# Optimization experiments

Hardware: AMD Instinct MI355X
Metric: run time of the kernel (lower is better)

Reference implementation:

```python
import jax, jax.numpy as jnp
import numpy as np

B, NX, NY, CIN = 4, 128, 128, 64
D, H = 64, 8  # out_channels, nhead
EPS = 1e-5


def setup_inputs() -> dict:
    key = jax.random.key(0)
    ks = jax.random.split(key, 12)
    s_in = 1.0 / np.sqrt(CIN)
    s_hd = 1.0 / np.sqrt(H * D)
    return {
        "v": jax.random.normal(ks[0], (B, NX, NY, CIN), jnp.float32),
        "Wq_w": jax.random.uniform(ks[1], (CIN, H * D), jnp.float32, -s_in, s_in),
        "Wq_b": jax.random.uniform(ks[2], (H * D,), jnp.float32, -s_in, s_in),
        "Wk_w": jax.random.uniform(ks[3], (CIN, H * D), jnp.float32, -s_in, s_in),
        "Wk_b": jax.random.uniform(ks[4], (H * D,), jnp.float32, -s_in, s_in),
        "Wv_w": jax.random.uniform(ks[5], (CIN, H * D), jnp.float32, -s_in, s_in),
        "Wv_b": jax.random.uniform(ks[6], (H * D,), jnp.float32, -s_in, s_in),
        "lnq_g": jnp.ones((H, D), jnp.float32),
        "lnq_b": jnp.zeros((H, D), jnp.float32),
        "lnk_g": jnp.ones((H, D), jnp.float32),
        "lnk_b": jnp.zeros((H, D), jnp.float32),
        "Wo_w": jax.random.uniform(ks[7], (H * D, D), jnp.float32, -s_hd, s_hd),
        "Wo_b": jax.random.uniform(ks[8], (D,), jnp.float32, -s_hd, s_hd),
    }


def _layernorm(x, gamma, beta):
    # x: [b,h,n,d]; gamma/beta: [h,d] (per-head params)
    mu = jnp.mean(x, axis=-1, keepdims=True)
    var = jnp.mean(jnp.square(x - mu), axis=-1, keepdims=True)
    xn = (x - mu) * jax.lax.rsqrt(var + EPS)
    return xn * gamma[None, :, None, :] + beta[None, :, None, :]


def reference(v, Wq_w, Wq_b, Wk_w, Wk_b, Wv_w, Wv_b,
              lnq_g, lnq_b, lnk_g, lnk_b, Wo_w, Wo_b):
    b, nx, ny, _ = v.shape
    n = nx * ny
    vf = v.reshape(b, n, -1)  # [b, n, cin]
    # QKV projections -> [b, h, n, d]
    def proj(w, bias):
        y = vf @ w + bias  # [b, n, h*d]
        return y.reshape(b, n, H, D).transpose(0, 2, 1, 3)
    Q = _layernorm(proj(Wq_w, Wq_b), lnq_g, lnq_b)
    K = _layernorm(proj(Wk_w, Wk_b), lnk_g, lnk_b)
    V = proj(Wv_w, Wv_b)
    # Non-softmax linear attention: (Q K^T) V == Q (K^T V); use O(n d^2) form
    kv = jnp.einsum('bhnd,bhne->bhde', K, V)      # [b,h,d,d]
    attn = jnp.einsum('bhmd,bhde->bhme', Q, kv)   # [b,h,n,d]
    attn = attn.transpose(0, 2, 1, 3).reshape(b, n, H * D)
    out = (attn @ Wo_w + Wo_b) / n
    return out.reshape(b, nx, ny, D)
```

## Files before the change

kernel.cpp:

```cpp
#include <hip/hip_runtime.h>
#include <hip/hip_bf16.h>

typedef __attribute__((ext_vector_type(8))) short bhalf8;
typedef __attribute__((ext_vector_type(4))) float f32x4;

#define MFMA_BF16 __builtin_amdgcn_mfma_f32_16x16x32_bf16

namespace {

constexpr int   NPIX  = 16384;
constexpr int   NCH   = 64;
constexpr int   TILE  = 66 * 64;
constexpr float EPSV  = 1e-5f;
constexpr float INV64 = 1.0f / 64.0f;
constexpr float INV_N = 1.0f / 16384.0f;

__device__ __forceinline__ unsigned short f2bf(float f) {
    unsigned int u = __builtin_bit_cast(unsigned int, f);
    u += 0x7fffu + ((u >> 16) & 1u);
    return (unsigned short)(u >> 16);
}

union B8 { bhalf8 v; unsigned int u[4]; };

__device__ __forceinline__ unsigned int pk2(float a, float b) {
    union { __hip_bfloat162 h; unsigned int u; } x;
    x.h = __float22bfloat162_rn(float2{a, b});
    return x.u;
}

__global__ void kpack(const float* __restrict__ Wk, const float* __restrict__ Wv,
                      const float* __restrict__ Wq,
                      unsigned short* __restrict__ wkpk, unsigned short* __restrict__ wvpk,
                      unsigned short* __restrict__ wqpk, unsigned short* __restrict__ wksumb,
                      float* __restrict__ cbeta)
{
    const int w = blockIdx.x >> 3, h = blockIdx.x & 7, t = threadIdx.x;
    const float* W = (w == 0) ? Wk : (w == 1) ? Wv : Wq;
    unsigned short* dst = (w == 0) ? wkpk : (w == 1) ? wvpk : wqpk;

    if (blockIdx.x == 0) cbeta[t] = 0.f;

#pragma unroll
    for (int i = 0; i < 2; ++i) {
        const int f = t * 2 + i;
        const int nt = (f >> 7) & 3, ks = (f >> 6) & 1, l = f & 63;
        const int g = l >> 4, m = l & 15;
        unsigned short tmp[8];
#pragma unroll
        for (int j = 0; j < 8; ++j)
            tmp[j] = f2bf(W[(size_t)(32 * ks + 8 * g + j) * 512 + h * 64 + 16 * nt + m]);
        unsigned short* d = dst + ((size_t)((h * 4 + nt) * 2 + ks)) * 512 + l * 8;
        *reinterpret_cast<ushort4*>(d)     = make_ushort4(tmp[0], tmp[1], tmp[2], tmp[3]);
        *reinterpret_cast<ushort4*>(d + 4) = make_ushort4(tmp[4], tmp[5], tmp[6], tmp[7]);
    }
    if (w == 0 && t < 64) {
        float s = 0.f;
        const float* row = Wk + (size_t)t * 512 + h * 64;
#pragma unroll
        for (int d = 0; d < 64; ++d) s += row[d];
        wksumb[h * 64 + t] = f2bf(s);
    }
}

__global__ __launch_bounds__(512, 2)
void ka_kv(const float* __restrict__ v,
           const unsigned short* __restrict__ wkpk, const unsigned short* __restrict__ wvpk,
           const unsigned short* __restrict__ wksumb,
           const float* __restrict__ bk, const float* __restrict__ bv,
           float* __restrict__ part)
{
    const int ch = blockIdx.x, b = blockIdx.y;
    const int t = threadIdx.x, h = t >> 6, l = t & 63, g = l >> 4, m16 = l & 15;

    __shared__ uint4 vlds4[2048];
    unsigned short* vlds = reinterpret_cast<unsigned short*>(vlds4);

    const float* vbase = v + ((size_t)b * NPIX + ch * 256) * 64;
#pragma unroll
    for (int i = 0; i < 4; ++i) {
        const int G = t + 512 * i;
        const int s = G >> 8, f = (G >> 6) & 3, ll = G & 63;
        const int mt = f >> 1, ks = f & 1, gg = ll >> 4, mm = ll & 15;
        const float* src = vbase + (size_t)(s * 32 + 16 * mt + mm) * 64 + 32 * ks + 8 * gg;
        const float4 a = *reinterpret_cast<const float4*>(src);
        const float4 c = *reinterpret_cast<const float4*>(src + 4);
        vlds4[G] = uint4{pk2(a.x, a.y), pk2(a.z, a.w), pk2(c.x, c.y), pk2(c.z, c.w)};
    }

    bhalf8 wkB[4][2], wvB[4][2], wks[2];
#pragma unroll
    for (int nt = 0; nt < 4; ++nt)
#pragma unroll
      for (int ks = 0; ks < 2; ++ks) {
          wkB[nt][ks] = *reinterpret_cast<const bhalf8*>(
              wkpk + ((size_t)((h * 4 + nt) * 2 + ks)) * 512 + l * 8);
          wvB[nt][ks] = *reinterpret_cast<const bhalf8*>(
              wvpk + ((size_t)((h * 4 + nt) * 2 + ks)) * 512 + l * 8);
      }
#pragma unroll
    for (int ks = 0; ks < 2; ++ks)
        wks[ks] = *reinterpret_cast<const bhalf8*>(wksumb + h * 64 + 32 * ks + 8 * g);

    float bksum;
    {
        float bl = bk[h * 64 + l];
#pragma unroll
        for (int m = 1; m < 64; m <<= 1) bl += __shfl_xor(bl, m, 64);
        bksum = bl;
    }
    float bkv[4], bvv[4];
#pragma unroll
    for (int nt = 0; nt < 4; ++nt) {
        bkv[nt] = bk[h * 64 + 16 * nt + m16];
        bvv[nt] = bv[h * 64 + 16 * nt + m16];
    }

    f32x4 kv[4][4];
#pragma unroll
    for (int i = 0; i < 4; ++i)
#pragma unroll
      for (int j = 0; j < 4; ++j) kv[i][j] = f32x4{0.f, 0.f, 0.f, 0.f};
    float tl[4] = {0.f, 0.f, 0.f, 0.f};
    float sv[4] = {0.f, 0.f, 0.f, 0.f};

    __syncthreads();

    for (int s = 0; s < 8; ++s) {
        bhalf8 vA[2][2];
#pragma unroll
        for (int mt = 0; mt < 2; ++mt)
#pragma unroll
          for (int ks = 0; ks < 2; ++ks)
            vA[mt][ks] = *reinterpret_cast<const bhalf8*>(
                vlds + ((size_t)(s * 4 + mt * 2 + ks) * 64 + l) * 8);

        f32x4 kq[2][4];
#pragma unroll
        for (int mt = 0; mt < 2; ++mt)
#pragma unroll
          for (int nt = 0; nt < 4; ++nt) {
              f32x4 a = {0.f, 0.f, 0.f, 0.f};
              a = MFMA_BF16(vA[mt][0], wkB[nt][0], a, 0, 0, 0);
              a = MFMA_BF16(vA[mt][1], wkB[nt][1], a, 0, 0, 0);
#pragma unroll
              for (int q = 0; q < 4; ++q) a[q] += bkv[nt];
              kq[mt][nt] = a;
          }
        f32x4 st[2];
#pragma unroll
        for (int mt = 0; mt < 2; ++mt) {
            f32x4 a = {0.f, 0.f, 0.f, 0.f};
            a = MFMA_BF16(vA[mt][0], wks[0], a, 0, 0, 0);
            a = MFMA_BF16(vA[mt][1], wks[1], a, 0, 0, 0);
            st[mt] = a;
        }
        f32x4 s2p[2];
#pragma unroll
        for (int mt = 0; mt < 2; ++mt)
#pragma unroll
          for (int q = 0; q < 4; ++q) {
              float acc = kq[mt][0][q] * kq[mt][0][q];
              acc = fmaf(kq[mt][1][q], kq[mt][1][q], acc);
              acc = fmaf(kq[mt][2][q], kq[mt][2][q], acc);
              acc = fmaf(kq[mt][3][q], kq[mt][3][q], acc);
              s2p[mt][q] = acc;
          }
#pragma unroll
        for (int mt = 0; mt < 2; ++mt)
#pragma unroll
          for (int q = 0; q < 4; ++q) {
              float x = s2p[mt][q];
              x += __shfl_xor(x, 1, 64);
              x += __shfl_xor(x, 2, 64);
              x += __shfl_xor(x, 4, 64);
              x += __shfl_xor(x, 8, 64);
              s2p[mt][q] = x;
          }
        f32x4 rsv[2], cmu[2];
#pragma unroll
        for (int mt = 0; mt < 2; ++mt)
#pragma unroll
          for (int q = 0; q < 4; ++q) {
              const float mu  = (st[mt][q] + bksum) * INV64;
              const float var = s2p[mt][q] * INV64 - mu * mu;
              const float rs  = rsqrtf(fmaxf(var, 0.f) + EPSV);
              rsv[mt][q] = rs;
              cmu[mt][q] = mu * rs;
          }
        B8 ka[4];
#pragma unroll
        for (int MT = 0; MT < 4; ++MT) {
            ka[MT].u[0] = pk2(kq[0][MT][0] * rsv[0][0], kq[0][MT][1] * rsv[0][1]);
            ka[MT].u[1] = pk2(kq[0][MT][2] * rsv[0][2], kq[0][MT][3] * rsv[0][3]);
            ka[MT].u[2] = pk2(kq[1][MT][0] * rsv[1][0], kq[1][MT][1] * rsv[1][1]);
            ka[MT].u[3] = pk2(kq[1][MT][2] * rsv[1][2], kq[1][MT][3] * rsv[1][3]);
        }
        f32x4 vq[2][4];
#pragma unroll
        for (int mt = 0; mt < 2; ++mt)
#pragma unroll
          for (int nt = 0; nt < 4; ++nt) {
              f32x4 a = {0.f, 0.f, 0.f, 0.f};
              a = MFMA_BF16(vA[mt][0], wvB[nt][0], a, 0, 0, 0);
              a = MFMA_BF16(vA[mt][1], wvB[nt][1], a, 0, 0, 0);
#pragma unroll
              for (int q = 0; q < 4; ++q) a[q] += bvv[nt];
              vq[mt][nt] = a;
          }
#pragma unroll
        for (int nt = 0; nt < 4; ++nt) {
            float acc = tl[nt], acc2 = sv[nt];
#pragma unroll
            for (int mt = 0; mt < 2; ++mt)
#pragma unroll
              for (int q = 0; q < 4; ++q) {
                  acc  = fmaf(cmu[mt][q], vq[mt][nt][q], acc);
                  acc2 += vq[mt][nt][q];
              }
            tl[nt] = acc; sv[nt] = acc2;
        }
        B8 vb[4];
#pragma unroll
        for (int NT = 0; NT < 4; ++NT) {
            vb[NT].u[0] = pk2(vq[0][NT][0], vq[0][NT][1]);
            vb[NT].u[1] = pk2(vq[0][NT][2], vq[0][NT][3]);
            vb[NT].u[2] = pk2(vq[1][NT][0], vq[1][NT][1]);
            vb[NT].u[3] = pk2(vq[1][NT][2], vq[1][NT][3]);
        }
#pragma unroll
        for (int MT = 0; MT < 4; ++MT)
#pragma unroll
          for (int NT = 0; NT < 4; ++NT)
              kv[MT][NT] = MFMA_BF16(ka[MT].v, vb[NT].v, kv[MT][NT], 0, 0, 0);
    }

#pragma unroll
    for (int nt = 0; nt < 4; ++nt) {
        float x = tl[nt];
        x += __shfl_xor(x, 16, 64); x += __shfl_xor(x, 32, 64);
        tl[nt] = x;
        float y = sv[nt];
        y += __shfl_xor(y, 16, 64); y += __shfl_xor(y, 32, 64);
        sv[nt] = y;
    }
    float* pdst = part + ((size_t)((b * NCH + ch) * 8 + h)) * TILE;
#pragma unroll
    for (int MT = 0; MT < 4; ++MT)
#pragma unroll
      for (int NT = 0; NT < 4; ++NT)
#pragma unroll
        for (int q = 0; q < 4; ++q)
            pdst[(16 * MT + 4 * g + q) * 64 + 16 * NT + m16] = kv[MT][NT][q];
    if (g == 0) {
#pragma unroll
        for (int nt = 0; nt < 4; ++nt) {
            pdst[64 * 64 + 16 * nt + m16] = tl[nt];
            pdst[65 * 64 + 16 * nt + m16] = sv[nt];
        }
    }
}

__global__ void k2a_reduce(const float* __restrict__ part, float* __restrict__ s2buf)
{
    const int seg = blockIdx.x, bh = blockIdx.y, t = threadIdx.x;
    const int b = bh >> 3, hh = bh & 7;
    const float* base = part + ((size_t)((b * NCH + seg * 8) * 8 + hh)) * TILE;
    float* dst = s2buf + ((size_t)(bh * 8 + seg)) * TILE;
#pragma unroll
    for (int k = 0; k < 5; ++k) {
        const int idx = t + k * 256;
        if (idx < TILE / 4) {
            float4 s = make_float4(0.f, 0.f, 0.f, 0.f);
#pragma unroll
            for (int i = 0; i < 8; ++i) {
                const float4 x = *reinterpret_cast<const float4*>(
                    base + (size_t)i * 8 * TILE + idx * 4);
                s.x += x.x; s.y += x.y; s.z += x.z; s.w += x.w;
            }
            *reinterpret_cast<float4*>(dst + idx * 4) = s;
        }
    }
}

__global__ void k2b_mix(const float* __restrict__ s2buf,
                        const float* __restrict__ lnkg, const float* __restrict__ lnkb,
                        const float* __restrict__ lnqg, const float* __restrict__ lnqb,
                        const float* __restrict__ Wo,   const float* __restrict__ Wob,
                        unsigned short* __restrict__ mpk, float* __restrict__ cbeta)
{
    const int h = blockIdx.x, b = blockIdx.y, t = threadIdx.x;
    __shared__ float kvs[64][65], wos[64][65], mls[64][65], Svs[64], tds[64], us[64];
    const int r = t >> 2, c0 = (t & 3) * 16;
    const float* sb = s2buf + ((size_t)((b * 8 + h) * 8)) * TILE;

    float acc[16];
#pragma unroll
    for (int i = 0; i < 16; ++i) acc[i] = 0.f;
#pragma unroll
    for (int seg = 0; seg < 8; ++seg) {
        const float* src = sb + (size_t)seg * TILE + r * 64 + c0;
#pragma unroll
        for (int q = 0; q < 4; ++q) {
            const float4 x = *reinterpret_cast<const float4*>(src + 4 * q);
            acc[4*q+0] += x.x; acc[4*q+1] += x.y; acc[4*q+2] += x.z; acc[4*q+3] += x.w;
        }
    }
#pragma unroll
    for (int i = 0; i < 16; ++i) kvs[r][c0 + i] = acc[i];

    if (t < 64) {
        float s = 0.f, s2 = 0.f;
#pragma unroll
        for (int seg = 0; seg < 8; ++seg) {
            s  += sb[(size_t)seg * TILE + 64 * 64 + t];
            s2 += sb[(size_t)seg * TILE + 65 * 64 + t];
        }
        tds[t] = s; Svs[t] = s2;
    }
#pragma unroll
    for (int i = 0; i < 16; i += 4) {
        const float4 x = *reinterpret_cast<const float4*>(
            Wo + ((size_t)(h * 64) + r) * 64 + c0 + i);
        wos[r][c0+i] = x.x; wos[r][c0+i+1] = x.y; wos[r][c0+i+2] = x.z; wos[r][c0+i+3] = x.w;
    }
    __syncthreads();
    {
        const float gk = lnkg[h * 64 + r], bk2 = lnkb[h * 64 + r];
#pragma unroll
        for (int i = 0; i < 16; ++i) {
            const int e = c0 + i;
            kvs[r][e] = gk * (kvs[r][e] - tds[e]) + bk2 * Svs[e];
        }
    }
    __syncthreads();
    if (t < 64) {
        float s = 0.f;
        for (int dd = 0; dd < 64; ++dd) s = fmaf(lnqb[h * 64 + dd], kvs[dd][t], s);
        us[t] = s;
    }
    float mrow[16];
#pragma unroll
    for (int i = 0; i < 16; ++i) mrow[i] = 0.f;
    for (int e2 = 0; e2 < 64; ++e2) {
        const float kr = kvs[r][e2];
#pragma unroll
        for (int i = 0; i < 16; ++i) mrow[i] = fmaf(kr, wos[e2][c0 + i], mrow[i]);
    }
    {
        const float gq = lnqg[h * 64 + r] * INV_N;
#pragma unroll
        for (int i = 0; i < 16; ++i) mls[r][c0 + i] = gq * mrow[i];
    }
    __syncthreads();
    if (t < 64) {
        float s = 0.f;
        for (int e2 = 0; e2 < 64; ++e2) s = fmaf(us[e2], wos[e2][t], s);
        atomicAdd(cbeta + b * 64 + t, s * INV_N);
        if (h == 0) atomicAdd(cbeta + b * 64 + t, Wob[t] * INV_N);
    }
#pragma unroll
    for (int i = 0; i < 2; ++i) {
        const int f = t * 2 + i;
        const int nt = (f >> 7) & 3, ks = (f >> 6) & 1, l = f & 63;
        const int g = l >> 4, m = l & 15;
        unsigned short o[8];
#pragma unroll
        for (int j = 0; j < 8; ++j) {
            const int d = 32 * ks + 16 * (j >> 2) + 4 * g + (j & 3);
            o[j] = f2bf(mls[d][16 * nt + m]);
        }
        unsigned short* dd = mpk + ((size_t)((b * 8 + h) * 8 + nt * 2 + ks)) * 512 + l * 8;
        *reinterpret_cast<ushort4*>(dd)     = make_ushort4(o[0], o[1], o[2], o[3]);
        *reinterpret_cast<ushort4*>(dd + 4) = make_ushort4(o[4], o[5], o[6], o[7]);
    }
}

__global__ __launch_bounds__(256, 2)
void k3_out(const float* __restrict__ v,
            const unsigned short* __restrict__ wqpk, const float* __restrict__ bq,
            const unsigned short* __restrict__ mpk,  const float* __restrict__ cbeta,
            float* __restrict__ out)
{
    const int blk = blockIdx.x, b = blockIdx.y;
    const int t = threadIdx.x, w = t >> 6, l = t & 63, g = l >> 4, m16 = l & 15;
    const size_t px0 = (size_t)b * NPIX + blk * 128 + w * 32;

    B8 vB[2][2];
#pragma unroll
    for (int nt = 0; nt < 2; ++nt)
#pragma unroll
      for (int ks = 0; ks < 2; ++ks) {
          const float* src = v + (px0 + 16 * nt + m16) * 64 + 32 * ks + 8 * g;
          const float4 a = *reinterpret_cast<const float4*>(src);
          const float4 c = *reinterpret_cast<const float4*>(src + 4);
          vB[nt][ks].u[0] = pk2(a.x, a.y); vB[nt][ks].u[1] = pk2(a.z, a.w);
          vB[nt][ks].u[2] = pk2(c.x, c.y); vB[nt][ks].u[3] = pk2(c.z, c.w);
      }
    float cbv[4];
#pragma unroll
    for (int nt = 0; nt < 4; ++nt) cbv[nt] = cbeta[b * 64 + 16 * nt + m16];

    f32x4 outa[2][4];
#pragma unroll
    for (int i = 0; i < 2; ++i)
#pragma unroll
      for (int j = 0; j < 4; ++j) outa[i][j] = f32x4{0.f, 0.f, 0.f, 0.f};

#pragma unroll
    for (int h = 0; h < 8; ++h) {
        bhalf8 wqA[4][2], mB[2][4];
#pragma unroll
        for (int mt = 0; mt < 4; ++mt)
#pragma unroll
          for (int ks = 0; ks < 2; ++ks)
            wqA[mt][ks] = *reinterpret_cast<const bhalf8*>(
                wqpk + ((size_t)((h * 4 + mt) * 2 + ks)) * 512 + l * 8);
#pragma unroll
        for (int ks = 0; ks < 2; ++ks)
#pragma unroll
          for (int nt = 0; nt < 4; ++nt)
            mB[ks][nt] = *reinterpret_cast<const bhalf8*>(
                mpk + ((size_t)((b * 8 + h) * 8 + nt * 2 + ks)) * 512 + l * 8);
        float4 bq4[4];
#pragma unroll
        for (int mt = 0; mt < 4; ++mt)
            bq4[mt] = *reinterpret_cast<const float4*>(bq + h * 64 + 16 * mt + 4 * g);

        f32x4 qa[4][2];
#pragma unroll
        for (int mt = 0; mt < 4; ++mt)
#pragma unroll
          for (int nt = 0; nt < 2; ++nt) {
              f32x4 a = {0.f, 0.f, 0.f, 0.f};
              a = MFMA_BF16(wqA[mt][0], vB[nt][0].v, a, 0, 0, 0);
              a = MFMA_BF16(wqA[mt][1], vB[nt][1].v, a, 0, 0, 0);
              a[0] += bq4[mt].x; a[1] += bq4[mt].y;
              a[2] += bq4[mt].z; a[3] += bq4[mt].w;
              qa[mt][nt] = a;
          }
        float mu[2], rs[2];
#pragma unroll
        for (int nt = 0; nt < 2; ++nt) {
            float s1 = 0.f, s2 = 0.f;
#pragma unroll
            for (int mt = 0; mt < 4; ++mt)
#pragma unroll
              for (int q = 0; q < 4; ++q) {
                  const float x = qa[mt][nt][q];
                  s1 += x; s2 = fmaf(x, x, s2);
              }
            s1 += __shfl_xor(s1, 16, 64); s1 += __shfl_xor(s1, 32, 64);
            s2 += __shfl_xor(s2, 16, 64); s2 += __shfl_xor(s2, 32, 64);
            mu[nt] = s1 * INV64;
            rs[nt] = rsqrtf(fmaxf(s2 * INV64 - mu[nt] * mu[nt], 0.f) + EPSV);
        }
        B8 ka[2][2];
#pragma unroll
        for (int MT = 0; MT < 2; ++MT)
#pragma unroll
          for (int ks = 0; ks < 2; ++ks) {
              ka[MT][ks].u[0] = pk2((qa[2*ks+0][MT][0] - mu[MT]) * rs[MT],
                                    (qa[2*ks+0][MT][1] - mu[MT]) * rs[MT]);
              ka[MT][ks].u[1] = pk2((qa[2*ks+0][MT][2] - mu[MT]) * rs[MT],
                                    (qa[2*ks+0][MT][3] - mu[MT]) * rs[MT]);
              ka[MT][ks].u[2] = pk2((qa[2*ks+1][MT][0] - mu[MT]) * rs[MT],
                                    (qa[2*ks+1][MT][1] - mu[MT]) * rs[MT]);
              ka[MT][ks].u[3] = pk2((qa[2*ks+1][MT][2] - mu[MT]) * rs[MT],
                                    (qa[2*ks+1][MT][3] - mu[MT]) * rs[MT]);
          }
#pragma unroll
        for (int MT = 0; MT < 2; ++MT)
#pragma unroll
          for (int nt = 0; nt < 4; ++nt) {
              outa[MT][nt] = MFMA_BF16(ka[MT][0].v, mB[0][nt], outa[MT][nt], 0, 0, 0);
              outa[MT][nt] = MFMA_BF16(ka[MT][1].v, mB[1][nt], outa[MT][nt], 0, 0, 0);
          }
    }

#pragma unroll
    for (int MT = 0; MT < 2; ++MT)
#pragma unroll
      for (int q = 0; q < 4; ++q) {
          float* orow = out + (px0 + 16 * MT + 4 * g + q) * 64;
#pragma unroll
          for (int nt = 0; nt < 4; ++nt)
              orow[16 * nt + m16] = outa[MT][nt][q] + cbv[nt];
      }
}

}

extern "C" void kernel_launch(void* const* d_in, const int* in_sizes, int n_in,
                              void* d_out, int out_size, void* d_ws, size_t ws_size,
                              hipStream_t stream)
{
    const float* v     = (const float*)d_in[0];
    const float* Wq_w  = (const float*)d_in[1];
    const float* Wq_b  = (const float*)d_in[2];
    const float* Wk_w  = (const float*)d_in[3];
    const float* Wk_b  = (const float*)d_in[4];
    const float* Wv_w  = (const float*)d_in[5];
    const float* Wv_b  = (const float*)d_in[6];
    const float* lnq_g = (const float*)d_in[7];
    const float* lnq_b = (const float*)d_in[8];
    const float* lnk_g = (const float*)d_in[9];
    const float* lnk_b = (const float*)d_in[10];
    const float* Wo_w  = (const float*)d_in[11];
    const float* Wo_b  = (const float*)d_in[12];
    float* out = (float*)d_out;

    float* wsf    = (float*)d_ws;
    float* part   = wsf;
    float* s2buf  = part + (size_t)4 * NCH * 8 * TILE;
    float* cbeta  = s2buf + (size_t)32 * 8 * TILE;
    unsigned short* base_s = (unsigned short*)(cbeta + 256);
    unsigned short* wkpk   = base_s;
    unsigned short* wvpk   = base_s + 32768;
    unsigned short* wqpk   = base_s + 65536;
    unsigned short* wksumb = base_s + 98304;
    unsigned short* mpk    = base_s + 98816;

    kpack<<<24, 256, 0, stream>>>(Wk_w, Wv_w, Wq_w, wkpk, wvpk, wqpk, wksumb, cbeta);
    ka_kv<<<dim3(NCH, 4), 512, 0, stream>>>(v, wkpk, wvpk, wksumb, Wk_b, Wv_b, part);
    k2a_reduce<<<dim3(8, 32), 256, 0, stream>>>(part, s2buf);
    k2b_mix<<<dim3(8, 4), 256, 0, stream>>>(s2buf, lnk_g, lnk_b, lnq_g, lnq_b,
                                            Wo_w, Wo_b, mpk, cbeta);
    k3_out<<<dim3(128, 4), 256, 0, stream>>>(v, wqpk, Wq_b, mpk, cbeta, out);
}
```

Before: 161.3 us.

## Fuse five kernel launches into one cooperative kernel with grid syncs

Merges the weight-packing, KV partial accumulation, reduction, mix and output stages into a single cooperative kernel of 256 blocks of 512 threads, separated by grid-wide barriers. This removes four kernel-launch gaps and the inter-kernel drain. The per-head bias contribution is now written to a per-(batch, head) buffer instead of being accumulated with atomics. In exchange, later stages run on a fixed grid of 256 blocks with 512 threads, which can reduce parallelism for stages such as the output pass that previously used 512 blocks of 256 threads. Each grid barrier also adds its own synchronisation cost.

```diff
diff --git a/kernel.cpp b/kernel.cpp
--- a/kernel.cpp
+++ b/kernel.cpp
@@ -1,5 +1,8 @@
 #include <hip/hip_runtime.h>
 #include <hip/hip_bf16.h>
+#include <hip/hip_cooperative_groups.h>
+
+namespace cg = cooperative_groups;
 
 typedef __attribute__((ext_vector_type(8))) short bhalf8;
 typedef __attribute__((ext_vector_type(4))) float f32x4;
@@ -29,464 +32,483 @@
     return x.u;
 }
 
-__global__ void kpack(const float* __restrict__ Wk, const float* __restrict__ Wv,
-                      const float* __restrict__ Wq,
-                      unsigned short* __restrict__ wkpk, unsigned short* __restrict__ wvpk,
-                      unsigned short* __restrict__ wqpk, unsigned short* __restrict__ wksumb,
-                      float* __restrict__ cbeta)
+__global__ __launch_bounds__(512, 2)
+void fused(const float* __restrict__ v,
+           const float* __restrict__ Wq, const float* __restrict__ bq,
+           const float* __restrict__ Wk, const float* __restrict__ bk,
+           const float* __restrict__ Wv, const float* __restrict__ bv,
+           const float* __restrict__ lnqg, const float* __restrict__ lnqb,
+           const float* __restrict__ lnkg, const float* __restrict__ lnkb,
+           const float* __restrict__ Wo,  const float* __restrict__ Wob,
+           float* __restrict__ out,
+           float* __restrict__ part, float* __restrict__ s2buf,
+           float* __restrict__ cbh,
+           unsigned short* __restrict__ wkpk, unsigned short* __restrict__ wvpk,
+           unsigned short* __restrict__ wqpk, unsigned short* __restrict__ wksumb,
+           unsigned short* __restrict__ mpk)
 {
-    const int w = blockIdx.x >> 3, h = blockIdx.x & 7, t = threadIdx.x;
-    const float* W = (w == 0) ? Wk : (w == 1) ? Wv : Wq;
-    unsigned short* dst = (w == 0) ? wkpk : (w == 1) ? wvpk : wqpk;
-
-    if (blockIdx.x == 0) cbeta[t] = 0.f;
-
-#pragma unroll
-    for (int i = 0; i < 2; ++i) {
-        const int f = t * 2 + i;
-        const int nt = (f >> 7) & 3, ks = (f >> 6) & 1, l = f & 63;
-        const int g = l >> 4, m = l & 15;
-        unsigned short tmp[8];
-#pragma unroll
-        for (int j = 0; j < 8; ++j)
-            tmp[j] = f2bf(W[(size_t)(32 * ks + 8 * g + j) * 512 + h * 64 + 16 * nt + m]);
-        unsigned short* d = dst + ((size_t)((h * 4 + nt) * 2 + ks)) * 512 + l * 8;
-        *reinterpret_cast<ushort4*>(d)     = make_ushort4(tmp[0], tmp[1], tmp[2], tmp[3]);
-        *reinterpret_cast<ushort4*>(d + 4) = make_ushort4(tmp[4], tmp[5], tmp[6], tmp[7]);
+    cg::grid_group grid = cg::this_grid();
+    const int bid = blockIdx.x, t = threadIdx.x;
+
+    __shared__ __align__(16) float smem[12864];
+
+    if (bid < 96) {
+        const int w = bid >> 5, sub = bid & 31, h = sub >> 2, nt = sub & 3;
+        const float* W = (w == 0) ? Wk : (w == 1) ? Wv : Wq;
+        unsigned short* dst = (w == 0) ? wkpk : (w == 1) ? wvpk : wqpk;
+        if (t < 128) {
+            const int ks = t >> 6, l = t & 63, g = l >> 4, m = l & 15;
+            unsigned short tmp[8];
+#pragma unroll
+            for (int j = 0; j < 8; ++j)
+                tmp[j] = f2bf(W[(size_t)(32 * ks + 8 * g + j) * 512 + h * 64 + 16 * nt + m]);
+            unsigned short* d = dst + ((size_t)((h * 4 + nt) * 2 + ks)) * 512 + l * 8;
+            *reinterpret_cast<ushort4*>(d)     = make_ushort4(tmp[0], tmp[1], tmp[2], tmp[3]);
+            *reinterpret_cast<ushort4*>(d + 4) = make_ushort4(tmp[4], tmp[5], tmp[6], tmp[7]);
+        }
+    } else if (bid < 104) {
+        const int h = bid - 96;
+        if (t < 64) {
+            float s = 0.f;
+            const float* row = Wk + (size_t)t * 512 + h * 64;
+#pragma unroll
+            for (int d = 0; d < 64; ++d) s += row[d];
+            wksumb[h * 64 + t] = f2bf(s);
+        }
     }
-    if (w == 0 && t < 64) {
-        float s = 0.f;
-        const float* row = Wk + (size_t)t * 512 + h * 64;
-#pragma unroll
-        for (int d = 0; d < 64; ++d) s += row[d];
-        wksumb[h * 64 + t] = f2bf(s);
+    __threadfence();
+    grid.sync();
+
+    {
+        const int b = bid >> 6, ch = bid & 63;
+        const int h = t >> 6, l = t & 63, g = l >> 4, m16 = l & 15;
+
+        uint4* vlds4 = reinterpret_cast<uint4*>(smem);
+        unsigned short* vlds = reinterpret_cast<unsigned short*>(smem);
+
+        const float* vbase = v + ((size_t)b * NPIX + ch * 256) * 64;
+#pragma unroll
+        for (int i = 0; i < 4; ++i) {
+            const int G = t + 512 * i;
+            const int s = G >> 8, f = (G >> 6) & 3, ll = G & 63;
+            const int mt = f >> 1, ks = f & 1, gg = ll >> 4, mm = ll & 15;
+            const float* src = vbase + (size_t)(s * 32 + 16 * mt + mm) * 64 + 32 * ks + 8 * gg;
+            const float4 a = *reinterpret_cast<const float4*>(src);
+            const float4 c = *reinterpret_cast<const float4*>(src + 4);
+            vlds4[G] = uint4{pk2(a.x, a.y), pk2(a.z, a.w), pk2(c.x, c.y), pk2(c.z, c.w)};
+        }
+
+        bhalf8 wkB[4][2], wvB[4][2], wks[2];
+#pragma unroll
+        for (int nt = 0; nt < 4; ++nt)
+#pragma unroll
+          for (int ks = 0; ks < 2; ++ks) {
+              wkB[nt][ks] = *reinterpret_cast<const bhalf8*>(
+                  wkpk + ((size_t)((h * 4 + nt) * 2 + ks)) * 512 + l * 8);
+              wvB[nt][ks] = *reinterpret_cast<const bhalf8*>(
+                  wvpk + ((size_t)((h * 4 + nt) * 2 + ks)) * 512 + l * 8);
+          }
+#pragma unroll
+        for (int ks = 0; ks < 2; ++ks)
+            wks[ks] = *reinterpret_cast<const bhalf8*>(wksumb + h * 64 + 32 * ks + 8 * g);
+
+        float bksum;
+        {
+            float bl = bk[h * 64 + l];
+#pragma unroll
+            for (int m = 1; m < 64; m <<= 1) bl += __shfl_xor(bl, m, 64);
+            bksum = bl;
+        }
+        float bkv[4], bvv[4];
+#pragma unroll
+        for (int nt = 0; nt < 4; ++nt) {
+            bkv[nt] = bk[h * 64 + 16 * nt + m16];
+            bvv[nt] = bv[h * 64 + 16 * nt + m16];
+        }
+
+        f32x4 kv[4][4];
+#pragma unroll
+        for (int i = 0; i < 4; ++i)
+#pragma unroll
+          for (int j = 0; j < 4; ++j) kv[i][j] = f32x4{0.f, 0.f, 0.f, 0.f};
+        float tl[4] = {0.f, 0.f, 0.f, 0.f};
+        float sv[4] = {0.f, 0.f, 0.f, 0.f};
+
+        __syncthreads();
+
+        for (int s = 0; s < 8; ++s) {
+            bhalf8 vA[2][2];
+#pragma unroll
+            for (int mt = 0; mt < 2; ++mt)
+#pragma unroll
+              for (int ks = 0; ks < 2; ++ks)
+                vA[mt][ks] = *reinterpret_cast<const bhalf8*>(
+                    vlds + ((size_t)(s * 4 + mt * 2 + ks) * 64 + l) * 8);
+
+            f32x4 kq[2][4];
+#pragma unroll
+            for (int mt = 0; mt < 2; ++mt)
+#pragma unroll
+              for (int nt = 0; nt < 4; ++nt) {
+                  f32x4 a = {0.f, 0.f, 0.f, 0.f};
+                  a = MFMA_BF16(vA[mt][0], wkB[nt][0], a, 0, 0, 0);
+                  a = MFMA_BF16(vA[mt][1], wkB[nt][1], a, 0, 0, 0);
+#pragma unroll
+                  for (int q = 0; q < 4; ++q) a[q] += bkv[nt];
+                  kq[mt][nt] = a;
+              }
+            f32x4 st[2];
+#pragma unroll
+            for (int mt = 0; mt < 2; ++mt) {
+                f32x4 a = {0.f, 0.f, 0.f, 0.f};
+                a = MFMA_BF16(vA[mt][0], wks[0], a, 0, 0, 0);
+                a = MFMA_BF16(vA[mt][1], wks[1], a, 0, 0, 0);
+                st[mt] = a;
+            }
+            f32x4 s2p[2];
+#pragma unroll
+            for (int mt = 0; mt < 2; ++mt)
+#pragma unroll
+              for (int q = 0; q < 4; ++q) {
+                  float acc = kq[mt][0][q] * kq[mt][0][q];
+                  acc = fmaf(kq[mt][1][q], kq[mt][1][q], acc);
+                  acc = fmaf(kq[mt][2][q], kq[mt][2][q], acc);
+                  acc = fmaf(kq[mt][3][q], kq[mt][3][q], acc);
+                  s2p[mt][q] = acc;
+              }
+#pragma unroll
+            for (int mt = 0; mt < 2; ++mt)
+#pragma unroll
+              for (int q = 0; q < 4; ++q) {
+                  float x = s2p[mt][q];
+                  x += __shfl_xor(x, 1, 64);
+                  x += __shfl_xor(x, 2, 64);
+                  x += __shfl_xor(x, 4, 64);
+                  x += __shfl_xor(x, 8, 64);
+                  s2p[mt][q] = x;
+              }
+            f32x4 rsv[2], cmu[2];
+#pragma unroll
+            for (int mt = 0; mt < 2; ++mt)
+#pragma unroll
+              for (int q = 0; q < 4; ++q) {
+                  const float mu  = (st[mt][q] + bksum) * INV64;
+                  const float var = s2p[mt][q] * INV64 - mu * mu;
+                  const float rs  = rsqrtf(fmaxf(var, 0.f) + EPSV);
+                  rsv[mt][q] = rs;
+                  cmu[mt][q] = mu * rs;
+              }
+            B8 ka[4];
+#pragma unroll
+            for (int MT = 0; MT < 4; ++MT) {
+                ka[MT].u[0] = pk2(kq[0][MT][0] * rsv[0][0], kq[0][MT][1] * rsv[0][1]);
+                ka[MT].u[1] = pk2(kq[0][MT][2] * rsv[0][2], kq[0][MT][3] * rsv[0][3]);
+                ka[MT].u[2] = pk2(kq[1][MT][0] * rsv[1][0], kq[1][MT][1] * rsv[1][1]);
+                ka[MT].u[3] = pk2(kq[1][MT][2] * rsv[1][2], kq[1][MT][3] * rsv[1][3]);
+            }
+            f32x4 vq[2][4];
+#pragma unroll
+            for (int mt = 0; mt < 2; ++mt)
+#pragma unroll
+              for (int nt = 0; nt < 4; ++nt) {
+                  f32x4 a = {0.f, 0.f, 0.f, 0.f};
+                  a = MFMA_BF16(vA[mt][0], wvB[nt][0], a, 0, 0, 0);
+                  a = MFMA_BF16(vA[mt][1], wvB[nt][1], a, 0, 0, 0);
+#pragma unroll
+                  for (int q = 0; q < 4; ++q) a[q] += bvv[nt];
+                  vq[mt][nt] = a;
+              }
+#pragma unroll
+            for (int nt = 0; nt < 4; ++nt) {
+                float acc = tl[nt], acc2 = sv[nt];
+#pragma unroll
+                for (int mt = 0; mt < 2; ++mt)
+#pragma unroll
+                  for (int q = 0; q < 4; ++q) {
+                      acc  = fmaf(cmu[mt][q], vq[mt][nt][q], acc);
+                      acc2 += vq[mt][nt][q];
+                  }
+                tl[nt] = acc; sv[nt] = acc2;
+            }
+            B8 vb[4];
+#pragma unroll
+            for (int NT = 0; NT < 4; ++NT) {
+                vb[NT].u[0] = pk2(vq[0][NT][0], vq[0][NT][1]);
+                vb[NT].u[1] = pk2(vq[0][NT][2], vq[0][NT][3]);
+                vb[NT].u[2] = pk2(vq[1][NT][0], vq[1][NT][1]);
+                vb[NT].u[3] = pk2(vq[1][NT][2], vq[1][NT][3]);
+            }
+#pragma unroll
+            for (int MT = 0; MT < 4; ++MT)
+#pragma unroll
+              for (int NT = 0; NT < 4; ++NT)
+                  kv[MT][NT] = MFMA_BF16(ka[MT].v, vb[NT].v, kv[MT][NT], 0, 0, 0);
+        }
+
+#pragma unroll
+        for (int nt = 0; nt < 4; ++nt) {
+            float x = tl[nt];
+            x += __shfl_xor(x, 16, 64); x += __shfl_xor(x, 32, 64);
+            tl[nt] = x;
+            float y = sv[nt];
+            y += __shfl_xor(y, 16, 64); y += __shfl_xor(y, 32, 64);
+            sv[nt] = y;
+        }
+        float* pdst = part + ((size_t)((b * NCH + ch) * 8 + h)) * TILE;
+#pragma unroll
+        for (int MT = 0; MT < 4; ++MT)
+#pragma unroll
+          for (int NT = 0; NT < 4; ++NT)
+#pragma unroll
+            for (int q = 0; q < 4; ++q)
+                pdst[(16 * MT + 4 * g + q) * 64 + 16 * NT + m16] = kv[MT][NT][q];
+        if (g == 0) {
+#pragma unroll
+            for (int nt = 0; nt < 4; ++nt) {
+                pdst[64 * 64 + 16 * nt + m16] = tl[nt];
+                pdst[65 * 64 + 16 * nt + m16] = sv[nt];
+            }
+        }
     }
-}
-
-__global__ __launch_bounds__(512, 2)
-void ka_kv(const float* __restrict__ v,
-           const unsigned short* __restrict__ wkpk, const unsigned short* __restrict__ wvpk,
-           const unsigned short* __restrict__ wksumb,
-           const float* __restrict__ bk, const float* __restrict__ bv,
-           float* __restrict__ part)
-{
-    const int ch = blockIdx.x, b = blockIdx.y;
-    const int t = threadIdx.x, h = t >> 6, l = t & 63, g = l >> 4, m16 = l & 15;
-
-    __shared__ uint4 vlds4[2048];
-    unsigned short* vlds = reinterpret_cast<unsigned short*>(vlds4);
-
-    const float* vbase = v + ((size_t)b * NPIX + ch * 256) * 64;
-#pragma unroll
-    for (int i = 0; i < 4; ++i) {
-        const int G = t + 512 * i;
-        const int s = G >> 8, f = (G >> 6) & 3, ll = G & 63;
-        const int mt = f >> 1, ks = f & 1, gg = ll >> 4, mm = ll & 15;
-        const float* src = vbase + (size_t)(s * 32 + 16 * mt + mm) * 64 + 32 * ks + 8 * gg;
-        const float4 a = *reinterpret_cast<const float4*>(src);
-        const float4 c = *reinterpret_cast<const float4*>(src + 4);
-        vlds4[G] = uint4{pk2(a.x, a.y), pk2(a.z, a.w), pk2(c.x, c.y), pk2(c.z, c.w)};
+    __threadfence();
+    grid.sync();
+
+    {
+        const int bh = bid >> 3, seg = bid & 7;
+        const int b = bh >> 3, hh = bh & 7;
+        const float* base = part + ((size_t)((b * NCH + seg * 8) * 8 + hh)) * TILE;
+        float* dst = s2buf + ((size_t)(bh * 8 + seg)) * TILE;
+#pragma unroll
+        for (int k = 0; k < 3; ++k) {
+            const int idx = t + k * 512;
+            if (idx < TILE / 4) {
+                float4 s = make_float4(0.f, 0.f, 0.f, 0.f);
+#pragma unroll
+                for (int i = 0; i < 8; ++i) {
+                    const float4 x = *reinterpret_cast<const float4*>(
+                        base + (size_t)i * 8 * TILE + idx * 4);
+                    s.x += x.x; s.y += x.y; s.z += x.z; s.w += x.w;
+                }
+                *reinterpret_cast<float4*>(dst + idx * 4) = s;
+            }
+        }
     }
-
-    bhalf8 wkB[4][2], wvB[4][2], wks[2];
-#pragma unroll
-    for (int nt = 0; nt < 4; ++nt)
-#pragma unroll
-      for (int ks = 0; ks < 2; ++ks) {
-          wkB[nt][ks] = *reinterpret_cast<const bhalf8*>(
-              wkpk + ((size_t)((h * 4 + nt) * 2 + ks)) * 512 + l * 8);
-          wvB[nt][ks] = *reinterpret_cast<const bhalf8*>(
-              wvpk + ((size_t)((h * 4 + nt) * 2 + ks)) * 512 + l * 8);
-      }
-#pragma unroll
-    for (int ks = 0; ks < 2; ++ks)
-        wks[ks] = *reinterpret_cast<const bhalf8*>(wksumb + h * 64 + 32 * ks + 8 * g);
-
-    float bksum;
+    __threadfence();
+    grid.sync();
+
+    if (bid < 32) {
+        const int h = bid & 7, b = bid >> 3;
+        float* kvs = smem;
+        float* wos = smem + 4160;
+        float* mls = smem + 8320;
+        float* Svs = smem + 12480;
+        float* tds = smem + 12544;
+        float* us  = smem + 12608;
+        const float* sb = s2buf + ((size_t)((b * 8 + h) * 8)) * TILE;
+
+        if (t < 256) {
+            const int r = t >> 2, c0 = (t & 3) * 16;
+            float acc[16];
+#pragma unroll
+            for (int i = 0; i < 16; ++i) acc[i] = 0.f;
+#pragma unroll
+            for (int seg = 0; seg < 8; ++seg) {
+                const float* src = sb + (size_t)seg * TILE + r * 64 + c0;
+#pragma unroll
+                for (int q = 0; q < 4; ++q) {
+                    const float4 x = *reinterpret_cast<const float4*>(src + 4 * q);
+                    acc[4*q+0] += x.x; acc[4*q+1] += x.y; acc[4*q+2] += x.z; acc[4*q+3] += x.w;
+                }
+            }
+#pragma unroll
+            for (int i = 0; i < 16; ++i) kvs[r * 65 + c0 + i] = acc[i];
+#pragma unroll
+            for (int i = 0; i < 16; i += 4) {
+                const float4 x = *reinterpret_cast<const float4*>(
+                    Wo + ((size_t)(h * 64) + r) * 64 + c0 + i);
+                wos[r * 65 + c0+i] = x.x; wos[r * 65 + c0+i+1] = x.y;
+                wos[r * 65 + c0+i+2] = x.z; wos[r * 65 + c0+i+3] = x.w;
+            }
+        }
+        if (t < 64) {
+            float s = 0.f, s2 = 0.f;
+#pragma unroll
+            for (int seg = 0; seg < 8; ++seg) {
+                s  += sb[(size_t)seg * TILE + 64 * 64 + t];
+                s2 += sb[(size_t)seg * TILE + 65 * 64 + t];
+            }
+            tds[t] = s; Svs[t] = s2;
+        }
+        __syncthreads();
+        if (t < 256) {
+            const int r = t >> 2, c0 = (t & 3) * 16;
+            const float gk = lnkg[h * 64 + r], bk2 = lnkb[h * 64 + r];
+#pragma unroll
+            for (int i = 0; i < 16; ++i) {
+                const int e = c0 + i;
+                kvs[r * 65 + e] = gk * (kvs[r * 65 + e] - tds[e]) + bk2 * Svs[e];
+            }
+        }
+        __syncthreads();
+        if (t < 64) {
+            float s = 0.f;
+            for (int dd = 0; dd < 64; ++dd) s = fmaf(lnqb[h * 64 + dd], kvs[dd * 65 + t], s);
+            us[t] = s;
+        }
+        if (t < 256) {
+            const int r = t >> 2, c0 = (t & 3) * 16;
+            float mrow[16];
+#pragma unroll
+            for (int i = 0; i < 16; ++i) mrow[i] = 0.f;
+            for (int e2 = 0; e2 < 64; ++e2) {
+                const float kr = kvs[r * 65 + e2];
+#pragma unroll
+                for (int i = 0; i < 16; ++i) mrow[i] = fmaf(kr, wos[e2 * 65 + c0 + i], mrow[i]);
+            }
+            const float gq = lnqg[h * 64 + r] * INV_N;
+#pragma unroll
+            for (int i = 0; i < 16; ++i) mls[r * 65 + c0 + i] = gq * mrow[i];
+        }
+        __syncthreads();
+        if (t < 64) {
+            float s = 0.f;
+            for (int e2 = 0; e2 < 64; ++e2) s = fmaf(us[e2], wos[e2 * 65 + t], s);
+            cbh[(size_t)(b * 8 + h) * 64 + t] = s * INV_N;
+        }
+        if (t < 256) {
+#pragma unroll
+            for (int i = 0; i < 2; ++i) {
+                const int f = t * 2 + i;
+                const int nt = (f >> 7) & 3, ks = (f >> 6) & 1, l = f & 63;
+                const int g = l >> 4, m = l & 15;
+                unsigned short o[8];
+#pragma unroll
+                for (int j = 0; j < 8; ++j) {
+                    const int d = 32 * ks + 16 * (j >> 2) + 4 * g + (j & 3);
+                    o[j] = f2bf(mls[d * 65 + 16 * nt + m]);
+                }
+                unsigned short* dd = mpk + ((size_t)((b * 8 + h) * 8 + nt * 2 + ks)) * 512 + l * 8;
+                *reinterpret_cast<ushort4*>(dd)     = make_ushort4(o[0], o[1], o[2], o[3]);
+                *reinterpret_cast<ushort4*>(dd + 4) = make_ushort4(o[4], o[5], o[6], o[7]);
+            }
+        }
+    }
+    __threadfence();
+    grid.sync();
+
     {
-        float bl = bk[h * 64 + l];
-#pragma unroll
-        for (int m = 1; m < 64; m <<= 1) bl += __shfl_xor(bl, m, 64);
-        bksum = bl;
-    }
-    float bkv[4], bvv[4];
-#pragma unroll
-    for (int nt = 0; nt < 4; ++nt) {
-        bkv[nt] = bk[h * 64 + 16 * nt + m16];
-        bvv[nt] = bv[h * 64 + 16 * nt + m16];
-    }
-
-    f32x4 kv[4][4];
-#pragma unroll
-    for (int i = 0; i < 4; ++i)
-#pragma unroll
-      for (int j = 0; j < 4; ++j) kv[i][j] = f32x4{0.f, 0.f, 0.f, 0.f};
-    float tl[4] = {0.f, 0.f, 0.f, 0.f};
-    float sv[4] = {0.f, 0.f, 0.f, 0.f};
-
-    __syncthreads();
-
-    for (int s = 0; s < 8; ++s) {
-        bhalf8 vA[2][2];
-#pragma unroll
-        for (int mt = 0; mt < 2; ++mt)
-#pragma unroll
-          for (int ks = 0; ks < 2; ++ks)
-            vA[mt][ks] = *reinterpret_cast<const bhalf8*>(
-                vlds + ((size_t)(s * 4 + mt * 2 + ks) * 64 + l) * 8);
-
-        f32x4 kq[2][4];
-#pragma unroll
-        for (int mt = 0; mt < 2; ++mt)
-#pragma unroll
-          for (int nt = 0; nt < 4; ++nt) {
-              f32x4 a = {0.f, 0.f, 0.f, 0.f};
-              a = MFMA_BF16(vA[mt][0], wkB[nt][0], a, 0, 0, 0);
-              a = MFMA_BF16(vA[mt][1], wkB[nt][1], a, 0, 0, 0);
-#pragma unroll
-              for (int q = 0; q < 4; ++q) a[q] += bkv[nt];
-              kq[mt][nt] = a;
+        const int b = bid >> 6, ch = bid & 63;
+        const int w = t >> 6, l = t & 63, g = l >> 4, m16 = l & 15;
+        const size_t px0 = (size_t)b * NPIX + ch * 256 + w * 32;
+
+        B8 vB[2][2];
+#pragma unroll
+        for (int nt = 0; nt < 2; ++nt)
+#pragma unroll
+          for (int ks = 0; ks < 2; ++ks) {
+              const float* src = v + (px0 + 16 * nt + m16) * 64 + 32 * ks + 8 * g;
+              const float4 a = *reinterpret_cast<const float4*>(src);
+              const float4 c = *reinterpret_cast<const float4*>(src + 4);
+              vB[nt][ks].u[0] = pk2(a.x, a.y); vB[nt][ks].u[1] = pk2(a.z, a.w);
+              vB[nt][ks].u[2] = pk2(c.x, c.y); vB[nt][ks].u[3] = pk2(c.z, c.w);
           }
-        f32x4 st[2];
-#pragma unroll
-        for (int mt = 0; mt < 2; ++mt) {
-            f32x4 a = {0.f, 0.f, 0.f, 0.f};
-            a = MFMA_BF16(vA[mt][0], wks[0], a, 0, 0, 0);
-            a = MFMA_BF16(vA[mt][1], wks[1], a, 0, 0, 0);
-            st[mt] = a;
-        }
-        f32x4 s2p[2];
-#pragma unroll
-        for (int mt = 0; mt < 2; ++mt)
+        float cbv[4];
+#pragma unroll
+        for (int nt = 0; nt < 4; ++nt) {
+            const int e = 16 * nt + m16;
+            float s = Wob[e] * INV_N;
+#pragma unroll
+            for (int h = 0; h < 8; ++h) s += cbh[(size_t)(b * 8 + h) * 64 + e];
+            cbv[nt] = s;
+        }
+
+        f32x4 outa[2][4];
+#pragma unroll
+        for (int i = 0; i < 2; ++i)
+#pragma unroll
+          for (int j = 0; j < 4; ++j) outa[i][j] = f32x4{0.f, 0.f, 0.f, 0.f};
+
+#pragma unroll
+        for (int h = 0; h < 8; ++h) {
+            bhalf8 wqA[4][2], mB[2][4];
+#pragma unroll
+            for (int mt = 0; mt < 4; ++mt)
+#pragma unroll
+              for (int ks = 0; ks < 2; ++ks)
+                wqA[mt][ks] = *reinterpret_cast<const bhalf8*>(
+                    wqpk + ((size_t)((h * 4 + mt) * 2 + ks)) * 512 + l * 8);
+#pragma unroll
+            for (int ks = 0; ks < 2; ++ks)
+#pragma unroll
+              for (int nt = 0; nt < 4; ++nt)
+                mB[ks][nt] = *reinterpret_cast<const bhalf8*>(
+                    mpk + ((size_t)((b * 8 + h) * 8 + nt * 2 + ks)) * 512 + l * 8);
+            float4 bq4[4];
+#pragma unroll
+            for (int mt = 0; mt < 4; ++mt)
+                bq4[mt] = *reinterpret_cast<const float4*>(bq + h * 64 + 16 * mt + 4 * g);
+
+            f32x4 qa[4][2];
+#pragma unroll
+            for (int mt = 0; mt < 4; ++mt)
+#pragma unroll
+              for (int nt = 0; nt < 2; ++nt) {
+                  f32x4 a = {0.f, 0.f, 0.f, 0.f};
+                  a = MFMA_BF16(wqA[mt][0], vB[nt][0].v, a, 0, 0, 0);
+                  a = MFMA_BF16(wqA[mt][1], vB[nt][1].v, a, 0, 0, 0);
+                  a[0] += bq4[mt].x; a[1] += bq4[mt].y;
+                  a[2] += bq4[mt].z; a[3] += bq4[mt].w;
+                  qa[mt][nt] = a;
+              }
+            float mu[2], rs[2];
+#pragma unroll
+            for (int nt = 0; nt < 2; ++nt) {
+                float s1 = 0.f, s2 = 0.f;
+#pragma unroll
+                for (int mt = 0; mt < 4; ++mt)
+#pragma unroll
+                  for (int q = 0; q < 4; ++q) {
+                      const float x = qa[mt][nt][q];
+                      s1 += x; s2 = fmaf(x, x, s2);
+                  }
+                s1 += __shfl_xor(s1, 16, 64); s1 += __shfl_xor(s1, 32, 64);
+                s2 += __shfl_xor(s2, 16, 64); s2 += __shfl_xor(s2, 32, 64);
+                mu[nt] = s1 * INV64;
+                rs[nt] = rsqrtf(fmaxf(s2 * INV64 - mu[nt] * mu[nt], 0.f) + EPSV);
+            }
+            B8 ka[2][2];
+#pragma unroll
+            for (int MT = 0; MT < 2; ++MT)
+#pragma unroll
+              for (int ks = 0; ks < 2; ++ks) {
+                  ka[MT][ks].u[0] = pk2((qa[2*ks+0][MT][0] - mu[MT]) * rs[MT],
+                                        (qa[2*ks+0][MT][1] - mu[MT]) * rs[MT]);
+                  ka[MT][ks].u[1] = pk2((qa[2*ks+0][MT][2] - mu[MT]) * rs[MT],
+                                        (qa[2*ks+0][MT][3] - mu[MT]) * rs[MT]);
+                  ka[MT][ks].u[2] = pk2((qa[2*ks+1][MT][0] - mu[MT]) * rs[MT],
+                                        (qa[2*ks+1][MT][1] - mu[MT]) * rs[MT]);
+                  ka[MT][ks].u[3] = pk2((qa[2*ks+1][MT][2] - mu[MT]) * rs[MT],
+                                        (qa[2*ks+1][MT][3] - mu[MT]) * rs[MT]);
+              }
+#pragma unroll
+            for (int MT = 0; MT < 2; ++MT)
+#pragma unroll
+              for (int nt = 0; nt < 4; ++nt) {
+                  outa[MT][nt] = MFMA_BF16(ka[MT][0].v, mB[0][nt], outa[MT][nt], 0, 0, 0);
+                  outa[MT][nt] = MFMA_BF16(ka[MT][1].v, mB[1][nt], outa[MT][nt], 0, 0, 0);
+              }
+        }
+
+#pragma unroll
+        for (int MT = 0; MT < 2; ++MT)
 #pragma unroll
           for (int q = 0; q < 4; ++q) {
-              float acc = kq[mt][0][q] * kq[mt][0][q];
-              acc = fmaf(kq[mt][1][q], kq[mt][1][q], acc);
-              acc = fmaf(kq[mt][2][q], kq[mt][2][q], acc);
-              acc = fmaf(kq[mt][3][q], kq[mt][3][q], acc);
-              s2p[mt][q] = acc;
-          }
-#pragma unroll
-        for (int mt = 0; mt < 2; ++mt)
-#pragma unroll
-          for (int q = 0; q < 4; ++q) {
-              float x = s2p[mt][q];
-              x += __shfl_xor(x, 1, 64);
-              x += __shfl_xor(x, 2, 64);
-              x += __shfl_xor(x, 4, 64);
-              x += __shfl_xor(x, 8, 64);
-              s2p[mt][q] = x;
-          }
-        f32x4 rsv[2], cmu[2];
-#pragma unroll
-        for (int mt = 0; mt < 2; ++mt)
-#pragma unroll
-          for (int q = 0; q < 4; ++q) {
-              const float mu  = (st[mt][q] + bksum) * INV64;
-              const float var = s2p[mt][q] * INV64 - mu * mu;
-              const float rs  = rsqrtf(fmaxf(var, 0.f) + EPSV);
-              rsv[mt][q] = rs;
-              cmu[mt][q] = mu * rs;
-          }
-        B8 ka[4];
-#pragma unroll
-        for (int MT = 0; MT < 4; ++MT) {
-            ka[MT].u[0] = pk2(kq[0][MT][0] * rsv[0][0], kq[0][MT][1] * rsv[0][1]);
-            ka[MT].u[1] = pk2(kq[0][MT][2] * rsv[0][2], kq[0][MT][3] * rsv[0][3]);
-            ka[MT].u[2] = pk2(kq[1][MT][0] * rsv[1][0], kq[1][MT][1] * rsv[1][1]);
-            ka[MT].u[3] = pk2(kq[1][MT][2] * rsv[1][2], kq[1][MT][3] * rsv[1][3]);
-        }
-        f32x4 vq[2][4];
-#pragma unroll
-        for (int mt = 0; mt < 2; ++mt)
-#pragma unroll
-          for (int nt = 0; nt < 4; ++nt) {
-              f32x4 a = {0.f, 0.f, 0.f, 0.f};
-              a = MFMA_BF16(vA[mt][0], wvB[nt][0], a, 0, 0, 0);
-              a = MFMA_BF16(vA[mt][1], wvB[nt][1], a, 0, 0, 0);
-#pragma unroll
-              for (int q = 0; q < 4; ++q) a[q] += bvv[nt];
-              vq[mt][nt] = a;
-          }
-#pragma unroll
-        for (int nt = 0; nt < 4; ++nt) {
-            float acc = tl[nt], acc2 = sv[nt];
-#pragma unroll
-            for (int mt = 0; mt < 2; ++mt)
-#pragma unroll
-              for (int q = 0; q < 4; ++q) {
-                  acc  = fmaf(cmu[mt][q], vq[mt][nt][q], acc);
-                  acc2 += vq[mt][nt][q];
-              }
-            tl[nt] = acc; sv[nt] = acc2;
-        }
-        B8 vb[4];
-#pragma unroll
-        for (int NT = 0; NT < 4; ++NT) {
-            vb[NT].u[0] = pk2(vq[0][NT][0], vq[0][NT][1]);
-            vb[NT].u[1] = pk2(vq[0][NT][2], vq[0][NT][3]);
-            vb[NT].u[2] = pk2(vq[1][NT][0], vq[1][NT][1]);
-            vb[NT].u[3] = pk2(vq[1][NT][2], vq[1][NT][3]);
-        }
-#pragma unroll
-        for (int MT = 0; MT < 4; ++MT)
-#pragma unroll
-          for (int NT = 0; NT < 4; ++NT)
-              kv[MT][NT] = MFMA_BF16(ka[MT].v, vb[NT].v, kv[MT][NT], 0, 0, 0);
-    }
-
-#pragma unroll
-    for (int nt = 0; nt < 4; ++nt) {
-        float x = tl[nt];
-        x += __shfl_xor(x, 16, 64); x += __shfl_xor(x, 32, 64);
-        tl[nt] = x;
-        float y = sv[nt];
-        y += __shfl_xor(y, 16, 64); y += __shfl_xor(y, 32, 64);
-        sv[nt] = y;
-    }
-    float* pdst = part + ((size_t)((b * NCH + ch) * 8 + h)) * TILE;
-#pragma unroll
-    for (int MT = 0; MT < 4; ++MT)
-#pragma unroll
-      for (int NT = 0; NT < 4; ++NT)
-#pragma unroll
-        for (int q = 0; q < 4; ++q)
-            pdst[(16 * MT + 4 * g + q) * 64 + 16 * NT + m16] = kv[MT][NT][q];
-    if (g == 0) {
-#pragma unroll
-        for (int nt = 0; nt < 4; ++nt) {
-            pdst[64 * 64 + 16 * nt + m16] = tl[nt];
-            pdst[65 * 64 + 16 * nt + m16] = sv[nt];
-        }
-    }
-}
-
-__global__ void k2a_reduce(const float* __restrict__ part, float* __restrict__ s2buf)
-{
-    const int seg = blockIdx.x, bh = blockIdx.y, t = threadIdx.x;
-    const int b = bh >> 3, hh = bh & 7;
-    const float* base = part + ((size_t)((b * NCH + seg * 8) * 8 + hh)) * TILE;
-    float* dst = s2buf + ((size_t)(bh * 8 + seg)) * TILE;
-#pragma unroll
-    for (int k = 0; k < 5; ++k) {
-        const int idx = t + k * 256;
-        if (idx < TILE / 4) {
-            float4 s = make_float4(0.f, 0.f, 0.f, 0.f);
-#pragma unroll
-            for (int i = 0; i < 8; ++i) {
-                const float4 x = *reinterpret_cast<const float4*>(
-                    base + (size_t)i * 8 * TILE + idx * 4);
-                s.x += x.x; s.y += x.y; s.z += x.z; s.w += x.w;
-            }
-            *reinterpret_cast<float4*>(dst + idx * 4) = s;
-        }
-    }
-}
-
-__global__ void k2b_mix(const float* __restrict__ s2buf,
-                        const float* __restrict__ lnkg, const float* __restrict__ lnkb,
-                        const float* __restrict__ lnqg, const float* __restrict__ lnqb,
-                        const float* __restrict__ Wo,   const float* __restrict__ Wob,
-                        unsigned short* __restrict__ mpk, float* __restrict__ cbeta)
-{
-    const int h = blockIdx.x, b = blockIdx.y, t = threadIdx.x;
-    __shared__ float kvs[64][65], wos[64][65], mls[64][65], Svs[64], tds[64], us[64];
-    const int r = t >> 2, c0 = (t & 3) * 16;
-    const float* sb = s2buf + ((size_t)((b * 8 + h) * 8)) * TILE;
-
-    float acc[16];
-#pragma unroll
-    for (int i = 0; i < 16; ++i) acc[i] = 0.f;
-#pragma unroll
-    for (int seg = 0; seg < 8; ++seg) {
-        const float* src = sb + (size_t)seg * TILE + r * 64 + c0;
-#pragma unroll
-        for (int q = 0; q < 4; ++q) {
-            const float4 x = *reinterpret_cast<const float4*>(src + 4 * q);
-            acc[4*q+0] += x.x; acc[4*q+1] += x.y; acc[4*q+2] += x.z; acc[4*q+3] += x.w;
-        }
-    }
-#pragma unroll
-    for (int i = 0; i < 16; ++i) kvs[r][c0 + i] = acc[i];
-
-    if (t < 64) {
-        float s = 0.f, s2 = 0.f;
-#pragma unroll
-        for (int seg = 0; seg < 8; ++seg) {
-            s  += sb[(size_t)seg * TILE + 64 * 64 + t];
-            s2 += sb[(size_t)seg * TILE + 65 * 64 + t];
-        }
-        tds[t] = s; Svs[t] = s2;
-    }
-#pragma unroll
-    for (int i = 0; i < 16; i += 4) {
-        const float4 x = *reinterpret_cast<const float4*>(
-            Wo + ((size_t)(h * 64) + r) * 64 + c0 + i);
-        wos[r][c0+i] = x.x; wos[r][c0+i+1] = x.y; wos[r][c0+i+2] = x.z; wos[r][c0+i+3] = x.w;
-    }
-    __syncthreads();
-    {
-        const float gk = lnkg[h * 64 + r], bk2 = lnkb[h * 64 + r];
-#pragma unroll
-        for (int i = 0; i < 16; ++i) {
-            const int e = c0 + i;
-            kvs[r][e] = gk * (kvs[r][e] - tds[e]) + bk2 * Svs[e];
-        }
-    }
-    __syncthreads();
-    if (t < 64) {
-        float s = 0.f;
-        for (int dd = 0; dd < 64; ++dd) s = fmaf(lnqb[h * 64 + dd], kvs[dd][t], s);
-        us[t] = s;
-    }
-    float mrow[16];
-#pragma unroll
-    for (int i = 0; i < 16; ++i) mrow[i] = 0.f;
-    for (int e2 = 0; e2 < 64; ++e2) {
-        const float kr = kvs[r][e2];
-#pragma unroll
-        for (int i = 0; i < 16; ++i) mrow[i] = fmaf(kr, wos[e2][c0 + i], mrow[i]);
-    }
-    {
-        const float gq = lnqg[h * 64 + r] * INV_N;
-#pragma unroll
-        for (int i = 0; i < 16; ++i) mls[r][c0 + i] = gq * mrow[i];
-    }
-    __syncthreads();
-    if (t < 64) {
-        float s = 0.f;
-        for (int e2 = 0; e2 < 64; ++e2) s = fmaf(us[e2], wos[e2][t], s);
-        atomicAdd(cbeta + b * 64 + t, s * INV_N);
-        if (h == 0) atomicAdd(cbeta + b * 64 + t, Wob[t] * INV_N);
-    }
-#pragma unroll
-    for (int i = 0; i < 2; ++i) {
-        const int f = t * 2 + i;
-        const int nt = (f >> 7) & 3, ks = (f >> 6) & 1, l = f & 63;
-        const int g = l >> 4, m = l & 15;
-        unsigned short o[8];
-#pragma unroll
-        for (int j = 0; j < 8; ++j) {
-            const int d = 32 * ks + 16 * (j >> 2) + 4 * g + (j & 3);
-            o[j] = f2bf(mls[d][16 * nt + m]);
-        }
-        unsigned short* dd = mpk + ((size_t)((b * 8 + h) * 8 + nt * 2 + ks)) * 512 + l * 8;
-        *reinterpret_cast<ushort4*>(dd)     = make_ushort4(o[0], o[1], o[2], o[3]);
-        *reinterpret_cast<ushort4*>(dd + 4) = make_ushort4(o[4], o[5], o[6], o[7]);
-    }
-}
-
-__global__ __launch_bounds__(256, 2)
-void k3_out(const float* __restrict__ v,
-            const unsigned short* __restrict__ wqpk, const float* __restrict__ bq,
-            const unsigned short* __restrict__ mpk,  const float* __restrict__ cbeta,
-            float* __restrict__ out)
-{
-    const int blk = blockIdx.x, b = blockIdx.y;
-    const int t = threadIdx.x, w = t >> 6, l = t & 63, g = l >> 4, m16 = l & 15;
-    const size_t px0 = (size_t)b * NPIX + blk * 128 + w * 32;
-
-    B8 vB[2][2];
-#pragma unroll
-    for (int nt = 0; nt < 2; ++nt)
-#pragma unroll
-      for (int ks = 0; ks < 2; ++ks) {
-          const float* src = v + (px0 + 16 * nt + m16) * 64 + 32 * ks + 8 * g;
-          const float4 a = *reinterpret_cast<const float4*>(src);
-          const float4 c = *reinterpret_cast<const float4*>(src + 4);
-          vB[nt][ks].u[0] = pk2(a.x, a.y); vB[nt][ks].u[1] = pk2(a.z, a.w);
-          vB[nt][ks].u[2] = pk2(c.x, c.y); vB[nt][ks].u[3] = pk2(c.z, c.w);
-      }
-    float cbv[4];
-#pragma unroll
-    for (int nt = 0; nt < 4; ++nt) cbv[nt] = cbeta[b * 64 + 16 * nt + m16];
-
-    f32x4 outa[2][4];
-#pragma unroll
-    for (int i = 0; i < 2; ++i)
-#pragma unroll
-      for (int j = 0; j < 4; ++j) outa[i][j] = f32x4{0.f, 0.f, 0.f, 0.f};
-
-#pragma unroll
-    for (int h = 0; h < 8; ++h) {
-        bhalf8 wqA[4][2], mB[2][4];
-#pragma unroll
-        for (int mt = 0; mt < 4; ++mt)
-#pragma unroll
-          for (int ks = 0; ks < 2; ++ks)
-            wqA[mt][ks] = *reinterpret_cast<const bhalf8*>(
-                wqpk + ((size_t)((h * 4 + mt) * 2 + ks)) * 512 + l * 8);
-#pragma unroll
-        for (int ks = 0; ks < 2; ++ks)
-#pragma unroll
-          for (int nt = 0; nt < 4; ++nt)
-            mB[ks][nt] = *reinterpret_cast<const bhalf8*>(
-                mpk + ((size_t)((b * 8 + h) * 8 + nt * 2 + ks)) * 512 + l * 8);
-        float4 bq4[4];
-#pragma unroll
-        for (int mt = 0; mt < 4; ++mt)
-            bq4[mt] = *reinterpret_cast<const float4*>(bq + h * 64 + 16 * mt + 4 * g);
-
-        f32x4 qa[4][2];
-#pragma unroll
-        for (int mt = 0; mt < 4; ++mt)
-#pragma unroll
-          for (int nt = 0; nt < 2; ++nt) {
-              f32x4 a = {0.f, 0.f, 0.f, 0.f};
-              a = MFMA_BF16(wqA[mt][0], vB[nt][0].v, a, 0, 0, 0);
-              a = MFMA_BF16(wqA[mt][1], vB[nt][1].v, a, 0, 0, 0);
-              a[0] += bq4[mt].x; a[1] += bq4[mt].y;
-              a[2] += bq4[mt].z; a[3] += bq4[mt].w;
-              qa[mt][nt] = a;
-          }
-        float mu[2], rs[2];
-#pragma unroll
-        for (int nt = 0; nt < 2; ++nt) {
-            float s1 = 0.f, s2 = 0.f;
-#pragma unroll
-            for (int mt = 0; mt < 4; ++mt)
-#pragma unroll
-              for (int q = 0; q < 4; ++q) {
-                  const float x = qa[mt][nt][q];
-                  s1 += x; s2 = fmaf(x, x, s2);
-              }
-            s1 += __shfl_xor(s1, 16, 64); s1 += __shfl_xor(s1, 32, 64);
-            s2 += __shfl_xor(s2, 16, 64); s2 += __shfl_xor(s2, 32, 64);
-            mu[nt] = s1 * INV64;
-            rs[nt] = rsqrtf(fmaxf(s2 * INV64 - mu[nt] * mu[nt], 0.f) + EPSV);
-        }
-        B8 ka[2][2];
-#pragma unroll
-        for (int MT = 0; MT < 2; ++MT)
-#pragma unroll
-          for (int ks = 0; ks < 2; ++ks) {
-              ka[MT][ks].u[0] = pk2((qa[2*ks+0][MT][0] - mu[MT]) * rs[MT],
-                                    (qa[2*ks+0][MT][1] - mu[MT]) * rs[MT]);
-              ka[MT][ks].u[1] = pk2((qa[2*ks+0][MT][2] - mu[MT]) * rs[MT],
-                                    (qa[2*ks+0][MT][3] - mu[MT]) * rs[MT]);
-              ka[MT][ks].u[2] = pk2((qa[2*ks+1][MT][0] - mu[MT]) * rs[MT],
-                                    (qa[2*ks+1][MT][1] - mu[MT]) * rs[MT]);
-              ka[MT][ks].u[3] = pk2((qa[2*ks+1][MT][2] - mu[MT]) * rs[MT],
-                                    (qa[2*ks+1][MT][3] - mu[MT]) * rs[MT]);
-          }
-#pragma unroll
-        for (int MT = 0; MT < 2; ++MT)
-#pragma unroll
-          for (int nt = 0; nt < 4; ++nt) {
-              outa[MT][nt] = MFMA_BF16(ka[MT][0].v, mB[0][nt], outa[MT][nt], 0, 0, 0);
-              outa[MT][nt] = MFMA_BF16(ka[MT][1].v, mB[1][nt], outa[MT][nt], 0, 0, 0);
+              float* orow = out + (px0 + 16 * MT + 4 * g + q) * 64;
+#pragma unroll
+              for (int nt = 0; nt < 4; ++nt)
+                  orow[16 * nt + m16] = outa[MT][nt][q] + cbv[nt];
           }
     }
-
-#pragma unroll
-    for (int MT = 0; MT < 2; ++MT)
-#pragma unroll
-      for (int q = 0; q < 4; ++q) {
-          float* orow = out + (px0 + 16 * MT + 4 * g + q) * 64;
-#pragma unroll
-          for (int nt = 0; nt < 4; ++nt)
-              orow[16 * nt + m16] = outa[MT][nt][q] + cbv[nt];
-      }
 }
 
 }
@@ -513,18 +535,25 @@
     float* wsf    = (float*)d_ws;
     float* part   = wsf;
     float* s2buf  = part + (size_t)4 * NCH * 8 * TILE;
-    float* cbeta  = s2buf + (size_t)32 * 8 * TILE;
-    unsigned short* base_s = (unsigned short*)(cbeta + 256);
+    float* cbh    = s2buf + (size_t)32 * 8 * TILE;
+    unsigned short* base_s = (unsigned short*)(cbh + 2048);
     unsigned short* wkpk   = base_s;
     unsigned short* wvpk   = base_s + 32768;
     unsigned short* wqpk   = base_s + 65536;
     unsigned short* wksumb = base_s + 98304;
     unsigned short* mpk    = base_s + 98816;
 
-    kpack<<<24, 256, 0, stream>>>(Wk_w, Wv_w, Wq_w, wkpk, wvpk, wqpk, wksumb, cbeta);
-    ka_kv<<<dim3(NCH, 4), 512, 0, stream>>>(v, wkpk, wvpk, wksumb, Wk_b, Wv_b, part);
-    k2a_reduce<<<dim3(8, 32), 256, 0, stream>>>(part, s2buf);
-    k2b_mix<<<dim3(8, 4), 256, 0, stream>>>(s2buf, lnk_g, lnk_b, lnq_g, lnq_b,
-                                            Wo_w, Wo_b, mpk, cbeta);
-    k3_out<<<dim3(128, 4), 256, 0, stream>>>(v, wqpk, Wq_b, mpk, cbeta, out);
+    void* args[] = {
+        (void*)&v,
+        (void*)&Wq_w, (void*)&Wq_b,
+        (void*)&Wk_w, (void*)&Wk_b,
+        (void*)&Wv_w, (void*)&Wv_b,
+        (void*)&lnq_g, (void*)&lnq_b,
+        (void*)&lnk_g, (void*)&lnk_b,
+        (void*)&Wo_w, (void*)&Wo_b,
+        (void*)&out,
+        (void*)&part, (void*)&s2buf, (void*)&cbh,
+        (void*)&wkpk, (void*)&wvpk, (void*)&wqpk, (void*)&wksumb, (void*)&mpk
+    };
+    hipLaunchCooperativeKernel(fused, dim3(256), dim3(512), args, 0, stream);
 }
```

Result: slower. 479.0 us (+196.9%).
